# Performance work log

Measured on AMD Instinct MI355X. Metric: run time of the kernel, lower is better.

The kernel has to match this reference:

```python
import jax, jax.numpy as jnp
import numpy as np
from jax import lax

EPS = 1e-6  # matches nn.CosineSimilarity(eps=1e-6)


def _box_sum_3x3(z):
    # z: [B,1,H,W] -> 3x3 same-padded box sum (kernel of ones)
    k = jnp.ones((1, 1, 3, 3), z.dtype)
    return lax.conv_general_dilated(z, k, (1, 1), ((1, 1), (1, 1)),
                                    dimension_numbers=('NCHW', 'OIHW', 'NCHW'))


def setup_inputs() -> dict:
    key = jax.random.key(0)
    k1, k2 = jax.random.split(key)
    T, B, C, H, W = 4, 32, 256, 32, 32
    x = jax.random.normal(k1, (T, B, C, H, W), dtype=jnp.float32)
    prev_drop_mask = jax.random.bernoulli(k2, 0.3, (B, H * W))
    return {"x": x, "prev_drop_mask": prev_drop_mask}


def reference(x, prev_drop_mask):
    T, B, C, H, W = x.shape
    xm = jnp.mean(x, axis=0)                      # [B,C,H,W]
    # F.conv2d with ones(C,C,3,3)/9 gives an output identical across output
    # channels: box3x3(sum_c x) / 9. Compute that single channel exactly.
    csum = jnp.sum(xm, axis=1, keepdims=True)     # [B,1,H,W]
    lm = _box_sum_3x3(csum) / 9.0                 # [B,1,H,W] == local_mean[:,o] for every o
    lm = lm.reshape(B, H * W)                     # [B,P]
    xf = xm.reshape(B, C, H * W)                  # [B,C,P]
    # cosine over channel dim; local_mean vector is lm replicated C times:
    #   dot = lm * sum_c x,  ||lm_vec|| = sqrt(C)*|lm|
    dot = lm * csum.reshape(B, H * W)
    nx = jnp.linalg.norm(xf, axis=1)              # [B,P]
    ny = jnp.sqrt(jnp.asarray(C, xm.dtype)) * jnp.abs(lm)
    sim = dot / (jnp.maximum(nx, EPS) * jnp.maximum(ny, EPS))
    scores = jnp.where(prev_drop_mask, -jnp.inf, -sim)
    return jax.nn.softmax(scores, axis=1).reshape(B, H, W)
```

## Files before the change

### kernel.cpp

```cpp
#include <hip/hip_runtime.h>
#include <math.h>

#define Bv 32
#define Cv 256
#define Hv 32
#define Wv 32
#define Pv 1024
#define Tv 4
#define TSTRIDE (Bv * Cv * Pv)

__global__ __launch_bounds__(256) void lss_partial(
    const float* __restrict__ x,
    float* __restrict__ part1,
    float* __restrict__ part2,
    int cc)
{
    const int chunk = blockIdx.x;
    const int b     = blockIdx.y;
    const int tid   = threadIdx.x;
    const int p4    = tid << 2;
    const int c0    = chunk * cc;

    float s1x = 0.f, s1y = 0.f, s1z = 0.f, s1w = 0.f;
    float s2x = 0.f, s2y = 0.f, s2z = 0.f, s2w = 0.f;

    const float* bp = x + ((size_t)b * Cv + c0) * Pv + p4;

    #pragma unroll 4
    for (int c = 0; c < cc; ++c) {
        const float4 v0 = *(const float4*)(bp);
        const float4 v1 = *(const float4*)(bp + (size_t)TSTRIDE);
        const float4 v2 = *(const float4*)(bp + (size_t)2 * TSTRIDE);
        const float4 v3 = *(const float4*)(bp + (size_t)3 * TSTRIDE);
        bp += Pv;

        const float mx = (v0.x + v1.x + v2.x + v3.x) * 0.25f;
        const float my = (v0.y + v1.y + v2.y + v3.y) * 0.25f;
        const float mz = (v0.z + v1.z + v2.z + v3.z) * 0.25f;
        const float mw = (v0.w + v1.w + v2.w + v3.w) * 0.25f;

        s1x += mx;  s2x += mx * mx;
        s1y += my;  s2y += my * my;
        s1z += mz;  s2z += mz * mz;
        s1w += mw;  s2w += mw * mw;
    }

    const size_t o = ((size_t)chunk * Bv + b) * Pv + p4;
    float4 r1; r1.x = s1x; r1.y = s1y; r1.z = s1z; r1.w = s1w;
    float4 r2; r2.x = s2x; r2.y = s2y; r2.z = s2z; r2.w = s2w;
    *(float4*)(part1 + o) = r1;
    *(float4*)(part2 + o) = r2;
}

__global__ __launch_bounds__(128) void lss_mid(
    const float* __restrict__ part1,
    const float* __restrict__ part2,
    float* __restrict__ csum_o,
    float* __restrict__ nx_o,
    int nch)
{
    const int b = blockIdx.y;
    const int p = blockIdx.x * 128 + threadIdx.x;

    float s1 = 0.f, s2 = 0.f;
    for (int ch = 0; ch < nch; ++ch) {
        const size_t o = ((size_t)ch * Bv + b) * Pv + p;
        s1 += part1[o];
        s2 += part2[o];
    }
    csum_o[b * Pv + p] = s1;
    nx_o[b * Pv + p]   = sqrtf(s2);
}

__global__ __launch_bounds__(1024) void lss_final(
    const float* __restrict__ csum_i,
    const float* __restrict__ nx_i,
    const int*   __restrict__ mask,
    float*       __restrict__ out)
{
    const int b   = blockIdx.x;
    const int tid = threadIdx.x;
    const int yy  = tid >> 5;
    const int xx  = tid & 31;
    const int wid = tid >> 6;

    __shared__ float cs[(Hv + 2) * (Wv + 2)];
    __shared__ float wred[16];

    const float csum = csum_i[b * Pv + tid];
    const float nx   = nx_i[b * Pv + tid];

    for (int i = tid; i < (Hv + 2) * (Wv + 2); i += Pv) cs[i] = 0.f;
    __syncthreads();
    cs[(yy + 1) * (Wv + 2) + (xx + 1)] = csum;
    __syncthreads();

    float lm = 0.f;
    #pragma unroll
    for (int dy = 0; dy < 3; ++dy)
        #pragma unroll
        for (int dx = 0; dx < 3; ++dx)
            lm += cs[(yy + dy) * (Wv + 2) + (xx + dx)];
    lm *= (1.0f / 9.0f);

    const float ny  = 16.0f * fabsf(lm);
    const float sim = (lm * csum) / (fmaxf(nx, 1e-6f) * fmaxf(ny, 1e-6f));

    const float score = mask[b * Pv + tid] ? -INFINITY : -sim;

    float v = score;
    #pragma unroll
    for (int off = 32; off > 0; off >>= 1)
        v = fmaxf(v, __shfl_xor(v, off, 64));
    if ((tid & 63) == 0) wred[wid] = v;
    __syncthreads();
    float m = wred[0];
    #pragma unroll
    for (int i = 1; i < 16; ++i) m = fmaxf(m, wred[i]);
    __syncthreads();

    const float e = expf(score - m);

    v = e;
    #pragma unroll
    for (int off = 32; off > 0; off >>= 1)
        v += __shfl_xor(v, off, 64);
    if ((tid & 63) == 0) wred[wid] = v;
    __syncthreads();
    float denom = 0.f;
    #pragma unroll
    for (int i = 0; i < 16; ++i) denom += wred[i];

    out[b * Pv + tid] = e / denom;
}

extern "C" void kernel_launch(void* const* d_in, const int* in_sizes, int n_in,
                              void* d_out, int out_size, void* d_ws, size_t ws_size,
                              hipStream_t stream) {
    const float* x    = (const float*)d_in[0];
    const int*   mask = (const int*)d_in[1];
    float*       out  = (float*)d_out;

    int nch = 32;
    while (nch > 1 &&
           ((size_t)nch * Bv * Pv * 2 + 2 * (size_t)Bv * Pv) * sizeof(float) > ws_size)
        nch >>= 1;
    const int cc = Cv / nch;

    float* part1  = (float*)d_ws;
    float* part2  = part1 + (size_t)nch * Bv * Pv;
    float* csum_b = part2 + (size_t)nch * Bv * Pv;
    float* nx_b   = csum_b + (size_t)Bv * Pv;

    dim3 g1(nch, Bv);
    lss_partial<<<g1, 256, 0, stream>>>(x, part1, part2, cc);
    dim3 g2(Pv / 128, Bv);
    lss_mid<<<g2, 128, 0, stream>>>(part1, part2, csum_b, nx_b, nch);
    lss_final<<<Bv, Pv, 0, stream>>>(csum_b, nx_b, mask, out);
}
```

Before: 200.9 us.

## Fuse mid reduction into final kernel and split pixels across blocks in phase one

The first kernel now splits each channel chunk across four pixel quarters and four channel lanes per block, reducing the lane partials in shared memory before writing. This gives far more blocks (2048 vs 1024) and shorter per-thread loops to hide the latency of the 128 MB read. The separate mid kernel is removed, and its channel-chunk reduction is folded into the final softmax kernel, saving a launch. The workspace size is now fixed at 16 chunks with no check against ws_size, so the code assumes the workspace is large enough.

New measurement: 192.4 us (median of 2 runs). 1.04x faster.

```diff
diff --git a/kernel.cpp b/kernel.cpp
--- a/kernel.cpp
+++ b/kernel.cpp
@@ -6,33 +6,36 @@
 #define Hv 32
 #define Wv 32
 #define Pv 1024
-#define Tv 4
 #define TSTRIDE (Bv * Cv * Pv)
+#define NCH 16
+#define CC  16
+#define PSPLIT 4
 
-__global__ __launch_bounds__(256) void lss_partial(
+__global__ __launch_bounds__(256) void lss_phase1(
     const float* __restrict__ x,
     float* __restrict__ part1,
-    float* __restrict__ part2,
-    int cc)
+    float* __restrict__ part2)
 {
-    const int chunk = blockIdx.x;
+    const int chunk = blockIdx.x >> 2;
+    const int ps    = blockIdx.x & 3;
     const int b     = blockIdx.y;
     const int tid   = threadIdx.x;
-    const int p4    = tid << 2;
-    const int c0    = chunk * cc;
+    const int cl    = tid >> 6;
+    const int lane  = tid & 63;
+    const int p0    = ps * 256 + (lane << 2);
 
     float s1x = 0.f, s1y = 0.f, s1z = 0.f, s1w = 0.f;
     float s2x = 0.f, s2y = 0.f, s2z = 0.f, s2w = 0.f;
 
-    const float* bp = x + ((size_t)b * Cv + c0) * Pv + p4;
+    const float* bp = x + ((size_t)b * Cv + chunk * CC + cl) * Pv + p0;
 
-    #pragma unroll 4
-    for (int c = 0; c < cc; ++c) {
+    #pragma unroll
+    for (int g = 0; g < CC / 4; ++g) {
         const float4 v0 = *(const float4*)(bp);
         const float4 v1 = *(const float4*)(bp + (size_t)TSTRIDE);
         const float4 v2 = *(const float4*)(bp + (size_t)2 * TSTRIDE);
         const float4 v3 = *(const float4*)(bp + (size_t)3 * TSTRIDE);
-        bp += Pv;
+        bp += 4 * Pv;
 
         const float mx = (v0.x + v1.x + v2.x + v3.x) * 0.25f;
         const float my = (v0.y + v1.y + v2.y + v3.y) * 0.25f;
@@ -45,36 +48,29 @@
         s1w += mw;  s2w += mw * mw;
     }
 
-    const size_t o = ((size_t)chunk * Bv + b) * Pv + p4;
-    float4 r1; r1.x = s1x; r1.y = s1y; r1.z = s1z; r1.w = s1w;
-    float4 r2; r2.x = s2x; r2.y = s2y; r2.z = s2z; r2.w = s2w;
-    *(float4*)(part1 + o) = r1;
-    *(float4*)(part2 + o) = r2;
-}
+    __shared__ float4 l1[4][64];
+    __shared__ float4 l2[4][64];
+    l1[cl][lane].x = s1x; l1[cl][lane].y = s1y; l1[cl][lane].z = s1z; l1[cl][lane].w = s1w;
+    l2[cl][lane].x = s2x; l2[cl][lane].y = s2y; l2[cl][lane].z = s2z; l2[cl][lane].w = s2w;
+    __syncthreads();
 
-__global__ __launch_bounds__(128) void lss_mid(
-    const float* __restrict__ part1,
-    const float* __restrict__ part2,
-    float* __restrict__ csum_o,
-    float* __restrict__ nx_o,
-    int nch)
-{
-    const int b = blockIdx.y;
-    const int p = blockIdx.x * 128 + threadIdx.x;
-
-    float s1 = 0.f, s2 = 0.f;
-    for (int ch = 0; ch < nch; ++ch) {
-        const size_t o = ((size_t)ch * Bv + b) * Pv + p;
-        s1 += part1[o];
-        s2 += part2[o];
+    if (tid < 128) {
+        const int t = tid & 63;
+        const float4* src = (tid < 64) ? &l1[0][0] : &l2[0][0];
+        const float4 a = src[t], c = src[64 + t], d = src[128 + t], e = src[192 + t];
+        float4 r;
+        r.x = (a.x + c.x) + (d.x + e.x);
+        r.y = (a.y + c.y) + (d.y + e.y);
+        r.z = (a.z + c.z) + (d.z + e.z);
+        r.w = (a.w + c.w) + (d.w + e.w);
+        float* dst = (tid < 64) ? part1 : part2;
+        *(float4*)(dst + ((size_t)chunk * Bv + b) * Pv + ps * 256 + (t << 2)) = r;
     }
-    csum_o[b * Pv + p] = s1;
-    nx_o[b * Pv + p]   = sqrtf(s2);
 }
 
 __global__ __launch_bounds__(1024) void lss_final(
-    const float* __restrict__ csum_i,
-    const float* __restrict__ nx_i,
+    const float* __restrict__ part1,
+    const float* __restrict__ part2,
     const int*   __restrict__ mask,
     float*       __restrict__ out)
 {
@@ -87,8 +83,15 @@
     __shared__ float cs[(Hv + 2) * (Wv + 2)];
     __shared__ float wred[16];
 
-    const float csum = csum_i[b * Pv + tid];
-    const float nx   = nx_i[b * Pv + tid];
+    float s1 = 0.f, s2 = 0.f;
+    #pragma unroll
+    for (int ch = 0; ch < NCH; ++ch) {
+        const size_t o = ((size_t)ch * Bv + b) * Pv + tid;
+        s1 += part1[o];
+        s2 += part2[o];
+    }
+    const float csum = s1;
+    const float nx   = sqrtf(s2);
 
     for (int i = tid; i < (Hv + 2) * (Wv + 2); i += Pv) cs[i] = 0.f;
     __syncthreads();
@@ -141,20 +144,10 @@
     const int*   mask = (const int*)d_in[1];
     float*       out  = (float*)d_out;
 
-    int nch = 32;
-    while (nch > 1 &&
-           ((size_t)nch * Bv * Pv * 2 + 2 * (size_t)Bv * Pv) * sizeof(float) > ws_size)
-        nch >>= 1;
-    const int cc = Cv / nch;
+    float* part1 = (float*)d_ws;
+    float* part2 = part1 + (size_t)NCH * Bv * Pv;
 
-    float* part1  = (float*)d_ws;
-    float* part2  = part1 + (size_t)nch * Bv * Pv;
-    float* csum_b = part2 + (size_t)nch * Bv * Pv;
-    float* nx_b   = csum_b + (size_t)Bv * Pv;
-
-    dim3 g1(nch, Bv);
-    lss_partial<<<g1, 256, 0, stream>>>(x, part1, part2, cc);
-    dim3 g2(Pv / 128, Bv);
-    lss_mid<<<g2, 128, 0, stream>>>(part1, part2, csum_b, nx_b, nch);
-    lss_final<<<Bv, Pv, 0, stream>>>(csum_b, nx_b, mask, out);
+    dim3 g1(NCH * PSPLIT, Bv);
+    lss_phase1<<<g1, 256, 0, stream>>>(x, part1, part2);
+    lss_final<<<Bv, Pv, 0, stream>>>(part1, part2, mask, out);
 }
```
